# Performance work log

Hardware: AMD Instinct MI355X
Metric: run time of the kernel (lower is better)

## Reference

```python
import jax, jax.numpy as jnp
import numpy as np

N, IN_F, OUT_F = 8192, 512, 64
ALPHA = 0.2  # leaky_relu negative slope


def setup_inputs() -> dict:
    key = jax.random.key(0)
    k1, k2, k3, k4 = jax.random.split(key, 4)
    h = jax.random.normal(k1, (N, IN_F), dtype=jnp.float32)
    adj = jax.random.uniform(k2, (N, N), dtype=jnp.float32)  # unused by the layer's math
    # fc: nn.Linear(in, out, bias=False) -> weight [out, in], xavier uniform
    limit = float(np.sqrt(6.0 / (IN_F + OUT_F)))
    W = jax.random.uniform(k3, (OUT_F, IN_F), minval=-limit, maxval=limit, dtype=jnp.float32)
    # a: Parameter [2*out, 1]; torch init is zeros then xavier in repo only for fc,
    # but zeros make attention uniform -> use small random for a meaningful baseline
    a = jax.random.normal(k4, (2 * OUT_F, 1), dtype=jnp.float32) * 0.1
    return {"h": h, "adj": adj, "W": W, "a": a}


def reference(h, adj, W, a):
    # Wh = fc(h): [N, F]
    Wh = h @ W.T
    F_ = Wh.shape[-1]
    # The torch code builds [N, N, 2F] of concat(Wh_i, Wh_j) and dots with a.
    # Identical math: e[i, j] = leaky_relu(Wh_i . a1 + Wh_j . a2)
    a1, a2 = a[:F_, 0], a[F_:, 0]          # each [F]
    s1 = Wh @ a1                            # [N]
    s2 = Wh @ a2                            # [N]
    e = jax.nn.leaky_relu(s1[:, None] + s2[None, :], ALPHA)  # [N, N]
    attention = jax.nn.softmax(e, axis=1)   # row-wise over neighbors j
    # dropout skipped (eval mode / training=False)
    return attention @ Wh                   # [N, F]
```

## Files before the change

### kernel.cpp

```cpp
#include <hip/hip_runtime.h>


constexpr int NV  = 8192;
constexpr int FIN = 512;
constexpr int NT  = 512;
constexpr int CH  = 32;
constexpr int NCH = 256;
constexpr int NBK = 4096;

__global__ __launch_bounds__(NT, 4) void k1_gemm(
    const float* __restrict__ h, const float* __restrict__ W,
    const float* __restrict__ a, float* __restrict__ Wh,
    float* __restrict__ s1, float* __restrict__ s2g)
{
    __shared__ float smem[8192];
    const int t = threadIdx.x, b = blockIdx.x;
    const int lane = t & 63, w = t >> 6;
    const int row0 = __builtin_amdgcn_readfirstlane(b * 16 + w * 2);
    float4 A0 = {0.f,0.f,0.f,0.f}, A1 = {0.f,0.f,0.f,0.f};
    const float4* Wf4 = reinterpret_cast<const float4*>(W);
    float4* S4 = reinterpret_cast<float4*>(smem);
    for (int pass = 0; pass < 4; ++pass) {
        #pragma unroll
        for (int it = 0; it < 4; ++it) {
            const int g = it * 512 + t;
            const int f = g >> 5, kk4 = g & 31;
            S4[kk4 * 64 + ((f + kk4) & 63)] = Wf4[f * 128 + pass * 32 + kk4];
        }
        __syncthreads();
        const float* hb = h + (size_t)row0 * FIN + pass * 128;
        #pragma unroll 8
        for (int k4 = 0; k4 < 32; ++k4) {
            const float4 wv = S4[k4 * 64 + ((lane + k4) & 63)];
            const float4 h0 = *reinterpret_cast<const float4*>(hb + k4 * 4);
            const float4 h1 = *reinterpret_cast<const float4*>(hb + FIN + k4 * 4);
            A0.x = fmaf(h0.x, wv.x, A0.x); A0.y = fmaf(h0.y, wv.y, A0.y);
            A0.z = fmaf(h0.z, wv.z, A0.z); A0.w = fmaf(h0.w, wv.w, A0.w);
            A1.x = fmaf(h1.x, wv.x, A1.x); A1.y = fmaf(h1.y, wv.y, A1.y);
            A1.z = fmaf(h1.z, wv.z, A1.z); A1.w = fmaf(h1.w, wv.w, A1.w);
        }
        __syncthreads();
    }
    const float acc0 = (A0.x + A0.y) + (A0.z + A0.w);
    const float acc1 = (A1.x + A1.y) + (A1.z + A1.w);
    Wh[(size_t)row0 * 64 + lane] = acc0;
    Wh[(size_t)(row0 + 1) * 64 + lane] = acc1;
    const float a1 = a[lane], a2 = a[64 + lane];
    float r0s1 = acc0 * a1, r0s2 = acc0 * a2;
    float r1s1 = acc1 * a1, r1s2 = acc1 * a2;
    #pragma unroll
    for (int off = 32; off > 0; off >>= 1) {
        r0s1 += __shfl_xor(r0s1, off);
        r0s2 += __shfl_xor(r0s2, off);
        r1s1 += __shfl_xor(r1s1, off);
        r1s2 += __shfl_xor(r1s2, off);
    }
    if (lane == 0) {
        s1[row0] = r0s1;     s2g[row0] = r0s2;
        s1[row0 + 1] = r1s1; s2g[row0 + 1] = r1s2;
    }
}

__device__ __forceinline__ int bucketOf(float x, float mu, float is) {
    const float c = erff((x - mu) * is * 0.70710678f);
    const int b = (int)((c * 0.5f + 0.5f) * 4096.0f);
    return min(max(b, 0), NBK - 1);
}

__global__ __launch_bounds__(NT, 1) void k2_out(
    const float* __restrict__ Wh, const float* __restrict__ s1,
    const float* __restrict__ s2g, float* __restrict__ out)
{
    __shared__ __align__(16) unsigned char pool[102784];
    float*          s2f  = reinterpret_cast<float*>(pool);
    unsigned*       Bst  = reinterpret_cast<unsigned*>(pool + 32768);
    unsigned short* sid  = reinterpret_cast<unsigned short*>(pool + 49152);
    float*          Us   = reinterpret_cast<float*>(pool + 65536);
    float*          Vp   = reinterpret_cast<float*>(pool + 81984);
    float*          sus  = reinterpret_cast<float*>(pool + 98432);
    float*          svp  = reinterpret_cast<float*>(pool + 99472);
    float*          segTU= reinterpret_cast<float*>(pool + 100512);
    float*          segTV= reinterpret_cast<float*>(pool + 101536);
    float*          segSU= reinterpret_cast<float*>(pool + 102560);
    float*          segSV= reinterpret_cast<float*>(pool + 102624);
    float*          fscr = reinterpret_cast<float*>(pool + 102688);
    unsigned*       uscr = reinterpret_cast<unsigned*>(pool + 102752);

    const int t = threadIdx.x, b = blockIdx.x;
    const int lane = t & 63, w = t >> 6;
    const int fq = b & 3;
    const int rg = b >> 2;

    float S = 0.f, SQ = 0.f;
    #pragma unroll
    for (int q = 0; q < 4; ++q) {
        const int idx = q * 2048 + t * 4;
        const float4 v = *reinterpret_cast<const float4*>(s2g + idx);
        *reinterpret_cast<float4*>(s2f + idx) = v;
        S += (v.x + v.y) + (v.z + v.w);
        SQ += (v.x*v.x + v.y*v.y) + (v.z*v.z + v.w*v.w);
    }
    #pragma unroll
    for (int off = 32; off > 0; off >>= 1) {
        S  += __shfl_xor(S, off);
        SQ += __shfl_xor(SQ, off);
    }
    if (lane == 0) { fscr[w] = S; fscr[8 + w] = SQ; }
    __syncthreads();
    float Stot = 0.f, SQtot = 0.f;
    #pragma unroll
    for (int q = 0; q < 8; ++q) { Stot += fscr[q]; SQtot += fscr[8 + q]; }
    const float mu = Stot * (1.f / NV);
    const float var = fmaxf(SQtot * (1.f / NV) - mu * mu, 1e-30f);
    const float isg = rsqrtf(var);

    #pragma unroll
    for (int e = 0; e < 8; ++e) Bst[t * 8 + e] = 0u;
    __syncthreads();
    #pragma unroll
    for (int q = 0; q < NV / NT; ++q) {
        const int j = q * NT + t;
        atomicAdd(&Bst[bucketOf(s2f[j], mu, isg)], 1u);
    }
    __syncthreads();

    {
        unsigned cnt[8]; unsigned tt = 0u;
        #pragma unroll
        for (int e = 0; e < 8; ++e) { cnt[e] = Bst[t * 8 + e]; tt += cnt[e]; }
        unsigned x = tt;
        #pragma unroll
        for (int d = 1; d < 64; d <<= 1) {
            const unsigned y = __shfl_up(x, d);
            if (lane >= d) x += y;
        }
        if (lane == 63) uscr[w] = x;
        __syncthreads();
        unsigned wb = 0u;
        for (int q = 0; q < 8; ++q) if (q < w) wb += uscr[q];
        unsigned run = wb + x - tt;
        #pragma unroll
        for (int e = 0; e < 8; ++e) { const unsigned c = cnt[e]; Bst[t * 8 + e] = run; run += c; }
    }
    __syncthreads();

    #pragma unroll
    for (int q = 0; q < NV / NT; ++q) {
        const int j = q * NT + t;
        const unsigned slot = atomicAdd(&Bst[bucketOf(s2f[j], mu, isg)], 1u);
        sid[slot] = (unsigned short)j;
    }
    __syncthreads();

    #pragma unroll
    for (int rep = 0; rep < 2; ++rep) {
        const int unit = rep * NT + t;
        const int c = unit >> 2;
        const int fs = (unit & 3) * 4;
        float au[4] = {0.f,0.f,0.f,0.f}, av[4] = {0.f,0.f,0.f,0.f};
        float su = 0.f, sv = 0.f;
        for (int q = 0; q < CH; ++q) {
            const int p = c * CH + q;
            const int j = sid[p];
            const float x = s2f[j];
            const float u = __expf(x);
            const float v = __expf(0.2f * x);
            const float4 wv = *reinterpret_cast<const float4*>(
                                  Wh + (size_t)j * 64 + fq * 16 + fs);
            au[0]=fmaf(u,wv.x,au[0]); au[1]=fmaf(u,wv.y,au[1]);
            au[2]=fmaf(u,wv.z,au[2]); au[3]=fmaf(u,wv.w,au[3]);
            av[0]=fmaf(v,wv.x,av[0]); av[1]=fmaf(v,wv.y,av[1]);
            av[2]=fmaf(v,wv.z,av[2]); av[3]=fmaf(v,wv.w,av[3]);
            su += u; sv += v;
        }
        *reinterpret_cast<float4*>(Us + c * 16 + fs) = make_float4(au[0],au[1],au[2],au[3]);
        *reinterpret_cast<float4*>(Vp + c * 16 + fs) = make_float4(av[0],av[1],av[2],av[3]);
        if ((unit & 3) == 0) { sus[c] = su; svp[c] = sv; }
    }
    __syncthreads();

    if (t < 256) {
        const int f = t & 15, seg = t >> 4;
        float run = 0.f;
        for (int q = 15; q >= 0; --q) {
            const int c = seg * 16 + q;
            run += Us[c * 16 + f];
            Us[c * 16 + f] = run;
        }
        segTU[seg * 16 + f] = run;
        float rv = 0.f;
        for (int q = 0; q < 16; ++q) {
            const int c = seg * 16 + q;
            const float tmp = Vp[c * 16 + f];
            Vp[c * 16 + f] = rv;
            rv += tmp;
        }
        segTV[seg * 16 + f] = rv;
    } else if (t < 272) {
        const int sg = t - 256;
        float r = 0.f;
        for (int q = 15; q >= 0; --q) { const int c = sg * 16 + q; r += sus[c]; sus[c] = r; }
        segSU[sg] = r;
        float rv = 0.f;
        for (int q = 0; q < 16; ++q) { const int c = sg * 16 + q; const float tmp = svp[c]; svp[c] = rv; rv += tmp; }
        segSV[sg] = rv;
    }
    __syncthreads();

    if (t < 256) {
        const int f = t & 15, seg = t >> 4;
        float offU = 0.f, offV = 0.f;
        for (int s = seg + 1; s < 16; ++s) offU += segTU[s * 16 + f];
        for (int s = 0; s < seg; ++s)      offV += segTV[s * 16 + f];
        for (int q = 0; q < 16; ++q) {
            const int c = seg * 16 + q;
            Us[c * 16 + f] += offU;
            Vp[c * 16 + f] += offV;
        }
    } else if (t < 272) {
        const int sg = t - 256;
        float oU = 0.f, oV = 0.f;
        for (int s = sg + 1; s < 16; ++s) oU += segSU[s];
        for (int s = 0; s < sg; ++s)      oV += segSV[s];
        for (int q = 0; q < 16; ++q) { sus[sg * 16 + q] += oU; svp[sg * 16 + q] += oV; }
    } else if (t < 288) {
        const int f = t - 272;
        Us[256 * 16 + f] = 0.f;
        float tot = 0.f;
        for (int s = 0; s < 16; ++s) tot += segTV[s * 16 + f];
        Vp[256 * 16 + f] = tot;
    } else if (t == 288) {
        float tv = 0.f;
        for (int s = 0; s < 16; ++s) tv += segSV[s];
        sus[256] = 0.f;
        svp[256] = tv;
    }
    __syncthreads();

    const int r = t >> 2, fs = (t & 3) * 4;
    const int i = rg * 128 + r;
    const float s1v = s1[i];
    const float thr = -s1v;
    const int bt = bucketOf(thr, mu, isg);
    const unsigned K0 = bt ? Bst[bt - 1] : 0u;
    const unsigned K1 = Bst[bt];
    const int c0   = (int)(K0 >> 5);
    const int cEnd = (int)((K1 + 31u) >> 5);
    float accU[4] = {0.f,0.f,0.f,0.f}, accV[4] = {0.f,0.f,0.f,0.f};
    float sau = 0.f, sav = 0.f;
    for (int p = c0 * CH; p < cEnd * CH; ++p) {
        const int j = sid[p];
        const float x = s2f[j];
        const float4 wv = *reinterpret_cast<const float4*>(
                              Wh + (size_t)j * 64 + fq * 16 + fs);
        const bool isV = ((unsigned)p < K0) | (((unsigned)p < K1) & (x <= thr));
        if (isV) {
            const float v = __expf(0.2f * x);
            accV[0]=fmaf(v,wv.x,accV[0]); accV[1]=fmaf(v,wv.y,accV[1]);
            accV[2]=fmaf(v,wv.z,accV[2]); accV[3]=fmaf(v,wv.w,accV[3]);
            sav += v;
        } else {
            const float u = __expf(x);
            accU[0]=fmaf(u,wv.x,accU[0]); accU[1]=fmaf(u,wv.y,accU[1]);
            accU[2]=fmaf(u,wv.z,accU[2]); accU[3]=fmaf(u,wv.w,accU[3]);
            sau += u;
        }
    }
    const float A  = __expf(s1v);
    const float Bc = __expf(0.2f * s1v);
    const float den = A * (sus[cEnd] + sau) + Bc * (svp[c0] + sav);
    const float inv = 1.f / den;
    float4 o;
    o.x = (A * (Us[cEnd*16 + fs+0] + accU[0]) + Bc * (Vp[c0*16 + fs+0] + accV[0])) * inv;
    o.y = (A * (Us[cEnd*16 + fs+1] + accU[1]) + Bc * (Vp[c0*16 + fs+1] + accV[1])) * inv;
    o.z = (A * (Us[cEnd*16 + fs+2] + accU[2]) + Bc * (Vp[c0*16 + fs+2] + accV[2])) * inv;
    o.w = (A * (Us[cEnd*16 + fs+3] + accU[3]) + Bc * (Vp[c0*16 + fs+3] + accV[3])) * inv;
    *reinterpret_cast<float4*>(out + (size_t)i * 64 + fq * 16 + fs) = o;
}

extern "C" void kernel_launch(void* const* d_in, const int* in_sizes, int n_in,
                              void* d_out, int out_size, void* d_ws, size_t ws_size,
                              hipStream_t stream) {
    (void)in_sizes; (void)n_in; (void)out_size; (void)ws_size;
    const float* h = (const float*)d_in[0];
    const float* W = (const float*)d_in[2];
    const float* a = (const float*)d_in[3];
    float* out = (float*)d_out;

    float* Wh  = (float*)d_ws;
    float* s1  = Wh + (size_t)NV * 64;
    float* s2g = s1 + NV;

    hipLaunchKernelGGL(k1_gemm, dim3(512), dim3(NT), 0, stream,
                       h, W, a, Wh, s1, s2g);
    hipLaunchKernelGGL(k2_out, dim3(256), dim3(NT), 0, stream,
                       Wh, s1, s2g, out);
}
```

Measured before the change: 51.28 us.

## Drop shared s2 copy, keep s2 in registers and raise k2 launch bounds

The 32 KB shared-memory copy of s2 is removed. Each thread keeps its 16 s2 values in registers for the histogram and scatter passes, and the gather loops read s2 from global memory instead. The launch bounds of k2_out go from 1 to 4 blocks per SM, and the Bst zeroing is merged into the first barrier, which saves one __syncthreads. The aim is a smaller LDS footprint for more resident blocks. In exchange, the gather loops take extra global-memory latency, and the tighter register cap may cause spills.

```diff
diff --git a/kernel.cpp b/kernel.cpp
--- a/kernel.cpp
+++ b/kernel.cpp
@@ -67,36 +67,32 @@
     return min(max(b, 0), NBK - 1);
 }
 
-__global__ __launch_bounds__(NT, 1) void k2_out(
+__global__ __launch_bounds__(NT, 4) void k2_out(
     const float* __restrict__ Wh, const float* __restrict__ s1,
     const float* __restrict__ s2g, float* __restrict__ out)
 {
-    __shared__ __align__(16) unsigned char pool[102784];
-    float*          s2f  = reinterpret_cast<float*>(pool);
-    unsigned*       Bst  = reinterpret_cast<unsigned*>(pool + 32768);
-    unsigned short* sid  = reinterpret_cast<unsigned short*>(pool + 49152);
-    float*          Us   = reinterpret_cast<float*>(pool + 65536);
-    float*          Vp   = reinterpret_cast<float*>(pool + 81984);
-    float*          sus  = reinterpret_cast<float*>(pool + 98432);
-    float*          svp  = reinterpret_cast<float*>(pool + 99472);
-    float*          segTU= reinterpret_cast<float*>(pool + 100512);
-    float*          segTV= reinterpret_cast<float*>(pool + 101536);
-    float*          segSU= reinterpret_cast<float*>(pool + 102560);
-    float*          segSV= reinterpret_cast<float*>(pool + 102624);
-    float*          fscr = reinterpret_cast<float*>(pool + 102688);
-    unsigned*       uscr = reinterpret_cast<unsigned*>(pool + 102752);
+    __shared__ unsigned       Bst[NBK];
+    __shared__ unsigned short sid[NV];
+    __shared__ float Us[257 * 16];
+    __shared__ float Vp[257 * 16];
+    __shared__ float sus[257];
+    __shared__ float svp[257];
+    __shared__ float segTU[256], segTV[256], segSU[16], segSV[16];
+    __shared__ float fscr[16];
+    __shared__ unsigned uscr[8];
 
     const int t = threadIdx.x, b = blockIdx.x;
     const int lane = t & 63, w = t >> 6;
     const int fq = b & 3;
     const int rg = b >> 2;
 
+    float xr[16];
     float S = 0.f, SQ = 0.f;
     #pragma unroll
     for (int q = 0; q < 4; ++q) {
-        const int idx = q * 2048 + t * 4;
-        const float4 v = *reinterpret_cast<const float4*>(s2g + idx);
-        *reinterpret_cast<float4*>(s2f + idx) = v;
+        const float4 v = *reinterpret_cast<const float4*>(s2g + q * 2048 + t * 4);
+        xr[q * 4 + 0] = v.x; xr[q * 4 + 1] = v.y;
+        xr[q * 4 + 2] = v.z; xr[q * 4 + 3] = v.w;
         S += (v.x + v.y) + (v.z + v.w);
         SQ += (v.x*v.x + v.y*v.y) + (v.z*v.z + v.w*v.w);
     }
@@ -106,6 +102,8 @@
         SQ += __shfl_xor(SQ, off);
     }
     if (lane == 0) { fscr[w] = S; fscr[8 + w] = SQ; }
+    #pragma unroll
+    for (int e = 0; e < 8; ++e) Bst[t * 8 + e] = 0u;
     __syncthreads();
     float Stot = 0.f, SQtot = 0.f;
     #pragma unroll
@@ -115,13 +113,8 @@
     const float isg = rsqrtf(var);
 
     #pragma unroll
-    for (int e = 0; e < 8; ++e) Bst[t * 8 + e] = 0u;
-    __syncthreads();
-    #pragma unroll
-    for (int q = 0; q < NV / NT; ++q) {
-        const int j = q * NT + t;
-        atomicAdd(&Bst[bucketOf(s2f[j], mu, isg)], 1u);
-    }
+    for (int q = 0; q < 16; ++q)
+        atomicAdd(&Bst[bucketOf(xr[q], mu, isg)], 1u);
     __syncthreads();
 
     {
@@ -145,10 +138,13 @@
     __syncthreads();
 
     #pragma unroll
-    for (int q = 0; q < NV / NT; ++q) {
-        const int j = q * NT + t;
-        const unsigned slot = atomicAdd(&Bst[bucketOf(s2f[j], mu, isg)], 1u);
-        sid[slot] = (unsigned short)j;
+    for (int q = 0; q < 4; ++q) {
+        #pragma unroll
+        for (int e = 0; e < 4; ++e) {
+            const int j = q * 2048 + t * 4 + e;
+            const unsigned slot = atomicAdd(&Bst[bucketOf(xr[q * 4 + e], mu, isg)], 1u);
+            sid[slot] = (unsigned short)j;
+        }
     }
     __syncthreads();
 
@@ -162,7 +158,7 @@
         for (int q = 0; q < CH; ++q) {
             const int p = c * CH + q;
             const int j = sid[p];
-            const float x = s2f[j];
+            const float x = s2g[j];
             const float u = __expf(x);
             const float v = __expf(0.2f * x);
             const float4 wv = *reinterpret_cast<const float4*>(
@@ -250,7 +246,7 @@
     float sau = 0.f, sav = 0.f;
     for (int p = c0 * CH; p < cEnd * CH; ++p) {
         const int j = sid[p];
-        const float x = s2f[j];
+        const float x = s2g[j];
         const float4 wv = *reinterpret_cast<const float4*>(
                               Wh + (size_t)j * 64 + fq * 16 + fs);
         const bool isV = ((unsigned)p < K0) | (((unsigned)p < K1) & (x <= thr));
```

Measured after the change: 65.52 us. 1.28x slower.
